# Performance work log

Measured on AMD Instinct MI355X. Metric: run time of the kernel, lower is better.

The kernel has to match this reference:

```python
import jax, jax.numpy as jnp
import numpy as np
import math

B, T, D, N = 4, 2048, 1024, 16
HD = D // N
SCALE = math.sqrt(D)  # source scales by sqrt(d_key) = sqrt(full model dim)
BIG = 1e9

def setup_inputs() -> dict:
    key = jax.random.key(0)
    ks = jax.random.split(key, 11)
    s = 1.0 / math.sqrt(D)
    return {
        "query": jax.random.normal(ks[0], (B, T, D), jnp.float32),
        "key": jax.random.normal(ks[1], (B, T, D), jnp.float32),
        "value": jax.random.normal(ks[2], (B, T, D), jnp.float32),
        "wq_w": jax.random.normal(ks[3], (D, D), jnp.float32) * s,
        "wq_b": jnp.zeros((D,), jnp.float32),
        "wk_w": jax.random.normal(ks[4], (D, D), jnp.float32) * s,
        "wk_b": jnp.zeros((D,), jnp.float32),
        "wv_w": jax.random.normal(ks[5], (D, D), jnp.float32) * s,
        "wv_b": jnp.zeros((D,), jnp.float32),
        "wo_w": jax.random.normal(ks[6], (D, D), jnp.float32) * s,
        "wo_b": jnp.zeros((D,), jnp.float32),
    }

def reference(query, key, value, wq_w, wq_b, wk_w, wk_b, wv_w, wv_b, wo_w, wo_b):
    # projections (torch Linear equiv; weights stored as (in,out))
    q = query @ wq_w + wq_b
    k = key @ wk_w + wk_b
    v = value @ wv_w + wv_b
    # split heads: (B,T,D) -> (B,N,T,HD)
    def split(x):
        return x.reshape(B, T, N, HD).transpose(0, 2, 1, 3)
    q, k, v = split(q), split(k), split(v)
    # dot products (source does elementwise mul+sum == einsum)
    scores = jnp.einsum('bnqd,bnkd->bnqk', q, k)
    # only_attend_front: subtract 1e9 on strict upper triangle
    tri = jnp.triu(jnp.ones((T, T), scores.dtype), 1) * BIG
    scores = scores - tri
    logits = scores / SCALE
    probs = jax.nn.softmax(logits, axis=-1)
    # zero rows where every position is masked (source trick)
    alive = ((scores <= -BIG / 2).sum(-1, keepdims=True) < T).astype(probs.dtype)
    probs = probs * alive
    out = jnp.einsum('bnqk,bnkd->bnqd', probs, v)  # (B,N,T,HD)
    out = out.transpose(0, 2, 1, 3).reshape(B, T, D)
    return out @ wo_w + wo_b
```

## Files before the change

### kernel.cpp

```cpp
#include <hip/hip_runtime.h>
#include <hip/hip_bf16.h>

#define BB 4
#define TT 2048
#define DD 1024
#define NHEAD 16
#define HDIM 64

typedef __bf16 v8bf __attribute__((ext_vector_type(8)));
typedef __bf16 v4bf __attribute__((ext_vector_type(4)));
typedef float  v4f  __attribute__((ext_vector_type(4)));

#define C2SCALE 0.04508422376f

__device__ __forceinline__ void gl2lds16(const void* g, void* l) {
  __builtin_amdgcn_global_load_lds(
      (__attribute__((address_space(1))) const void*)g,
      (__attribute__((address_space(3))) void*)l, 16, 0, 0);
}

__global__ __launch_bounds__(256) void prep(
    const float* __restrict__ qsrc, const float* __restrict__ ksrc,
    const float* __restrict__ vsrc,
    const float* __restrict__ w0, const float* __restrict__ w1,
    const float* __restrict__ w2, const float* __restrict__ w3,
    __bf16* __restrict__ qdst, __bf16* __restrict__ kdst,
    __bf16* __restrict__ vdst,
    __bf16* __restrict__ t0, __bf16* __restrict__ t1,
    __bf16* __restrict__ t2, __bf16* __restrict__ t3) {
  constexpr int STR = 72;
  __shared__ __bf16 sh[64 * STR];
  int bx = blockIdx.x, tid = threadIdx.x;
  if (bx < 12288) {
    const float* src = bx < 4096 ? qsrc : bx < 8192 ? ksrc : vsrc;
    __bf16* dst = bx < 4096 ? qdst : bx < 8192 ? kdst : vdst;
    int i = (bx & 4095) * 256 + tid;
    const float4* s = (const float4*)src + (size_t)i * 2;
    float4 f0 = s[0], f1 = s[1];
    v8bf v;
    v[0] = (__bf16)f0.x; v[1] = (__bf16)f0.y; v[2] = (__bf16)f0.z; v[3] = (__bf16)f0.w;
    v[4] = (__bf16)f1.x; v[5] = (__bf16)f1.y; v[6] = (__bf16)f1.z; v[7] = (__bf16)f1.w;
    *(v8bf*)(dst + (size_t)i * 8) = v;
  } else {
    int idx = bx - 12288;
    int z = idx >> 8;
    const float* W = z == 0 ? w0 : z == 1 ? w1 : z == 2 ? w2 : w3;
    __bf16* Wt = z == 0 ? t0 : z == 1 ? t1 : z == 2 ? t2 : t3;
    int n0 = (idx & 15) * 64, k0 = ((idx >> 4) & 15) * 64;
#pragma unroll
    for (int p = 0; p < 4; ++p) {
      int c = tid + p * 256;
      int r = c >> 4, off = (c & 15) * 4;
      float4 f = *(const float4*)(W + (size_t)(k0 + r) * DD + n0 + off);
      __bf16* d = &sh[r * STR + off];
      d[0] = (__bf16)f.x; d[1] = (__bf16)f.y; d[2] = (__bf16)f.z; d[3] = (__bf16)f.w;
    }
    __syncthreads();
#pragma unroll
    for (int p = 0; p < 2; ++p) {
      int c = tid + p * 256;
      int nr = c >> 3, koff = (c & 7) * 8;
      v8bf v;
#pragma unroll
      for (int j = 0; j < 8; ++j) v[j] = sh[(koff + j) * STR + nr];
      *(v8bf*)(Wt + (size_t)(n0 + nr) * DD + k0 + koff) = v;
    }
  }
}

__device__ __forceinline__ void gemm_core(const __bf16* __restrict__ A,
                                          const __bf16* __restrict__ Wt,
                                          int m0, int n0,
                                          __bf16* ash, __bf16* bsh,
                                          int wave, int lane, int quad, int l15,
                                          v4f acc[4][4]) {
  int wm = (wave & 1) * 64, wn = (wave >> 1) * 64;
  for (int k0 = 0; k0 < DD; k0 += 64) {
    __syncthreads();
#pragma unroll
    for (int i = 0; i < 4; ++i) {
      int c = wave * 256 + i * 64 + lane;
      int row = c >> 3, g = (c & 7) ^ (row & 7);
      gl2lds16(A + (size_t)(m0 + row) * DD + k0 + g * 8, ash + wave * 2048 + i * 512);
      gl2lds16(Wt + (size_t)(n0 + row) * DD + k0 + g * 8, bsh + wave * 2048 + i * 512);
    }
    __syncthreads();
#pragma unroll
    for (int ks = 0; ks < 2; ++ks) {
      int sw = (((ks * 4 + quad) ^ (l15 & 7))) * 8;
      v8bf a[4], b[4];
#pragma unroll
      for (int jm = 0; jm < 4; ++jm) a[jm] = *(v8bf*)&ash[(wm + jm * 16 + l15) * 64 + sw];
#pragma unroll
      for (int jn = 0; jn < 4; ++jn) b[jn] = *(v8bf*)&bsh[(wn + jn * 16 + l15) * 64 + sw];
#pragma unroll
      for (int jm = 0; jm < 4; ++jm)
#pragma unroll
        for (int jn = 0; jn < 4; ++jn)
          acc[jm][jn] = __builtin_amdgcn_mfma_f32_16x16x32_bf16(a[jm], b[jn], acc[jm][jn], 0, 0, 0);
    }
  }
}

__device__ __forceinline__ void swz_tiles(int& m0, int& n0) {
  int lin = blockIdx.x + 8 * blockIdx.y;
  int c = lin & 7, t = lin >> 3;
  n0 = (t & 7) * 128;
  m0 = (c + ((t >> 3) << 3)) * 128;
}

__global__ __launch_bounds__(256) void gemm_qkv(
    const __bf16* __restrict__ Qc, const __bf16* __restrict__ Kc,
    const __bf16* __restrict__ Vc,
    const __bf16* __restrict__ wqT, const __bf16* __restrict__ wkT,
    const __bf16* __restrict__ wvT,
    const float* __restrict__ qb, const float* __restrict__ kb,
    const float* __restrict__ vb,
    __bf16* __restrict__ Qp, __bf16* __restrict__ Kp, __bf16* __restrict__ VTb) {
  __shared__ __bf16 ash[128 * 64];
  __shared__ __bf16 bsh[128 * 64];
  int z = blockIdx.z;
  const __bf16* A  = z == 0 ? Qc : z == 1 ? Kc : Vc;
  const __bf16* Wt = z == 0 ? wqT : z == 1 ? wkT : wvT;
  const float* bias = z == 0 ? qb : z == 1 ? kb : vb;
  int tid = threadIdx.x, wave = tid >> 6, lane = tid & 63;
  int quad = lane >> 4, l15 = lane & 15;
  int m0, n0;
  swz_tiles(m0, n0);
  int wm = (wave & 1) * 64, wn = (wave >> 1) * 64;
  v4f acc[4][4];
#pragma unroll
  for (int jm = 0; jm < 4; ++jm)
#pragma unroll
    for (int jn = 0; jn < 4; ++jn) acc[jm][jn] = (v4f){0.f, 0.f, 0.f, 0.f};

  gemm_core(A, Wt, m0, n0, ash, bsh, wave, lane, quad, l15, acc);

  if (z == 2) {
    int b = m0 >> 11;
    int tbase = (m0 & 2047) + wm;
#pragma unroll
    for (int jn = 0; jn < 4; ++jn) {
      int col = n0 + wn + jn * 16 + l15;
      float bv = bias[col];
      __bf16* rowp = VTb + ((size_t)(b * 16 + (col >> 6)) * 64 + (col & 63)) * TT;
#pragma unroll
      for (int jm = 0; jm < 4; ++jm) {
        v4bf o;
#pragma unroll
        for (int r = 0; r < 4; ++r) o[r] = (__bf16)(acc[jm][jn][r] + bv);
        *(v4bf*)(rowp + tbase + jm * 16 + quad * 4) = o;
      }
    }
  } else {
    __bf16* C = z == 0 ? Qp : Kp;
    float scale = z == 0 ? C2SCALE : 1.0f;
#pragma unroll
    for (int jn = 0; jn < 4; ++jn) {
      int col = n0 + wn + jn * 16 + l15;
      float bv = bias[col];
#pragma unroll
      for (int jm = 0; jm < 4; ++jm) {
#pragma unroll
        for (int r = 0; r < 4; ++r) {
          int row = m0 + wm + jm * 16 + quad * 4 + r;
          C[(size_t)row * DD + col] = (__bf16)((acc[jm][jn][r] + bv) * scale);
        }
      }
    }
  }
}

__global__ __launch_bounds__(256) void gemm_out(const __bf16* __restrict__ A,
                                                const __bf16* __restrict__ Wt,
                                                const float* __restrict__ bias,
                                                float* __restrict__ C) {
  __shared__ __bf16 ash[128 * 64];
  __shared__ __bf16 bsh[128 * 64];
  int tid = threadIdx.x, wave = tid >> 6, lane = tid & 63;
  int quad = lane >> 4, l15 = lane & 15;
  int m0, n0;
  swz_tiles(m0, n0);
  int wm = (wave & 1) * 64, wn = (wave >> 1) * 64;
  v4f acc[4][4];
#pragma unroll
  for (int jm = 0; jm < 4; ++jm)
#pragma unroll
    for (int jn = 0; jn < 4; ++jn) acc[jm][jn] = (v4f){0.f, 0.f, 0.f, 0.f};

  gemm_core(A, Wt, m0, n0, ash, bsh, wave, lane, quad, l15, acc);

#pragma unroll
  for (int jn = 0; jn < 4; ++jn) {
    int col = n0 + wn + jn * 16 + l15;
    float bv = bias[col];
#pragma unroll
    for (int jm = 0; jm < 4; ++jm) {
#pragma unroll
      for (int r = 0; r < 4; ++r) {
        int row = m0 + wm + jm * 16 + quad * 4 + r;
        C[(size_t)row * DD + col] = acc[jm][jn][r] + bv;
      }
    }
  }
}

__global__ __launch_bounds__(256) void attn_bal(const __bf16* __restrict__ Q,
                                                const __bf16* __restrict__ K,
                                                const __bf16* __restrict__ VT,
                                                __bf16* __restrict__ O) {
  __shared__ __bf16 ksh[2][64 * 64];
  __shared__ __bf16 vsh[2][64 * 64];
  __shared__ __bf16 psh[128 * 64];
  int tid = threadIdx.x, wave = tid >> 6, lane = tid & 63;
  int quad = lane >> 4, l15 = lane & 15;
  int swz = l15 & 7;
  int lin = blockIdx.x + 8 * blockIdx.y;
  int c = lin & 7, t = lin >> 3;
  int xq = t & 7;
  int bh = c + ((t >> 3) << 3);
  int b = bh >> 4, h = bh & 15;
  const __bf16* Qb = Q + (size_t)(b * TT) * DD + h * HDIM;
  const __bf16* Kb = K + (size_t)(b * TT) * DD + h * HDIM;
  const __bf16* Vb = VT + (size_t)bh * HDIM * TT;
  __bf16* Ob = O + (size_t)(b * TT) * DD + h * HDIM;

  v8bf ones;
#pragma unroll
  for (int j = 0; j < 8; ++j) ones[j] = (__bf16)1.0f;

  for (int phase = 0; phase < 2; ++phase) {
    int qi = phase ? 15 - xq : xq;
    int q0 = qi * 128;
    int ktiles = 2 * qi + 2;

#pragma unroll
    for (int i = 0; i < 4; ++i) {
      int cc = wave * 256 + i * 64 + lane;
      int row = cc >> 3, g = (cc & 7) ^ (row & 7);
      gl2lds16(Qb + (size_t)(q0 + row) * DD + g * 8, psh + wave * 2048 + i * 512);
    }
#pragma unroll
    for (int i = 0; i < 2; ++i) {
      int cc = wave * 128 + i * 64 + lane;
      int row = cc >> 3, g = (cc & 7) ^ (row & 7);
      gl2lds16(Kb + (size_t)row * DD + g * 8, &ksh[0][wave * 1024 + i * 512]);
      gl2lds16(Vb + (size_t)row * TT + g * 8, &vsh[0][wave * 1024 + i * 512]);
    }
    __builtin_amdgcn_s_waitcnt(0);
    __syncthreads();

    v8bf qf[2][2];
#pragma unroll
    for (int set = 0; set < 2; ++set)
#pragma unroll
      for (int ks = 0; ks < 2; ++ks)
        qf[set][ks] = *(v8bf*)&psh[(wave * 32 + set * 16 + l15) * 64 + ((ks * 4 + quad) ^ swz) * 8];

    int qg[2] = {q0 + wave * 32 + l15, q0 + wave * 32 + 16 + l15};
    v4f oacc[2][4], lracc[2];
#pragma unroll
    for (int set = 0; set < 2; ++set) {
      lracc[set] = (v4f){0.f, 0.f, 0.f, 0.f};
#pragma unroll
      for (int jm = 0; jm < 4; ++jm) oacc[set][jm] = (v4f){0.f, 0.f, 0.f, 0.f};
    }

    int pbuf = 0;
    for (int kt = 0; kt < ktiles; ++kt) {
      if (kt + 1 < ktiles) {
        int k0n = (kt + 1) * 64;
#pragma unroll
        for (int i = 0; i < 2; ++i) {
          int cc = wave * 128 + i * 64 + lane;
          int row = cc >> 3, g = (cc & 7) ^ (row & 7);
          gl2lds16(Kb + (size_t)(k0n + row) * DD + g * 8, &ksh[pbuf ^ 1][wave * 1024 + i * 512]);
          gl2lds16(Vb + (size_t)row * TT + k0n + g * 8, &vsh[pbuf ^ 1][wave * 1024 + i * 512]);
        }
      }
      int k0 = kt * 64;
      const __bf16* kshp = &ksh[pbuf][0];
      const __bf16* vshp = &vsh[pbuf][0];

      v4f s[2][4];
#pragma unroll
      for (int set = 0; set < 2; ++set)
#pragma unroll
        for (int jf = 0; jf < 4; ++jf) s[set][jf] = (v4f){0.f, 0.f, 0.f, 0.f};
#pragma unroll
      for (int ks = 0; ks < 2; ++ks) {
        int sw = ((ks * 4 + quad) ^ swz) * 8;
#pragma unroll
        for (int jf = 0; jf < 4; ++jf) {
          v8bf kf = *(v8bf*)&kshp[(jf * 16 + l15) * 64 + sw];
          s[0][jf] = __builtin_amdgcn_mfma_f32_16x16x32_bf16(kf, qf[0][ks], s[0][jf], 0, 0, 0);
          s[1][jf] = __builtin_amdgcn_mfma_f32_16x16x32_bf16(kf, qf[1][ks], s[1][jf], 0, 0, 0);
        }
      }

      bool diag = (kt >= 2 * qi);
#pragma unroll
      for (int set = 0; set < 2; ++set) {
        int qrow = wave * 32 + set * 16 + l15;
        __bf16* prow = &psh[qrow * 64];
#pragma unroll
        for (int jf = 0; jf < 4; ++jf) {
          v4bf pk;
#pragma unroll
          for (int r = 0; r < 4; ++r) {
            float p = __builtin_amdgcn_exp2f(s[set][jf][r]);
            if (diag) {
              int kg = k0 + jf * 16 + quad * 4 + r;
              if (kg > qg[set]) p = 0.f;
            }
            pk[r] = (__bf16)p;
          }
          int chunk = jf * 2 + (quad >> 1);
          *(v4bf*)&prow[(chunk ^ swz) * 8 + (quad & 1) * 4] = pk;
        }
      }

#pragma unroll
      for (int ks = 0; ks < 2; ++ks) {
        int sw = ((ks * 4 + quad) ^ swz) * 8;
        v8bf pb0 = *(v8bf*)&psh[(wave * 32 + l15) * 64 + sw];
        v8bf pb1 = *(v8bf*)&psh[(wave * 32 + 16 + l15) * 64 + sw];
        lracc[0] = __builtin_amdgcn_mfma_f32_16x16x32_bf16(ones, pb0, lracc[0], 0, 0, 0);
        lracc[1] = __builtin_amdgcn_mfma_f32_16x16x32_bf16(ones, pb1, lracc[1], 0, 0, 0);
#pragma unroll
        for (int jm = 0; jm < 4; ++jm) {
          v8bf vf = *(v8bf*)&vshp[(jm * 16 + l15) * 64 + sw];
          oacc[0][jm] = __builtin_amdgcn_mfma_f32_16x16x32_bf16(vf, pb0, oacc[0][jm], 0, 0, 0);
          oacc[1][jm] = __builtin_amdgcn_mfma_f32_16x16x32_bf16(vf, pb1, oacc[1][jm], 0, 0, 0);
        }
      }

      __builtin_amdgcn_s_waitcnt(0);
      __syncthreads();
      pbuf ^= 1;
    }

#pragma unroll
    for (int set = 0; set < 2; ++set) {
      float inv = 1.0f / lracc[set][0];
      int q = q0 + wave * 32 + set * 16 + l15;
#pragma unroll
      for (int jm = 0; jm < 4; ++jm) {
        v4bf o;
#pragma unroll
        for (int r = 0; r < 4; ++r) o[r] = (__bf16)(oacc[set][jm][r] * inv);
        *(v4bf*)(Ob + (size_t)q * DD + jm * 16 + quad * 4) = o;
      }
    }
  }
}

extern "C" void kernel_launch(void* const* d_in, const int* in_sizes, int n_in,
                              void* d_out, int out_size, void* d_ws, size_t ws_size,
                              hipStream_t stream) {
  const float* query = (const float*)d_in[0];
  const float* key_  = (const float*)d_in[1];
  const float* value = (const float*)d_in[2];
  const float* wq_w = (const float*)d_in[3];
  const float* wq_b = (const float*)d_in[4];
  const float* wk_w = (const float*)d_in[5];
  const float* wk_b = (const float*)d_in[6];
  const float* wv_w = (const float*)d_in[7];
  const float* wv_b = (const float*)d_in[8];
  const float* wo_w = (const float*)d_in[9];
  const float* wo_b = (const float*)d_in[10];

  char* ws = (char*)d_ws;
  const size_t MB = (size_t)1 << 20;
  __bf16* wqT = (__bf16*)(ws + 0 * MB);
  __bf16* wkT = (__bf16*)(ws + 2 * MB);
  __bf16* wvT = (__bf16*)(ws + 4 * MB);
  __bf16* woT = (__bf16*)(ws + 6 * MB);
  __bf16* Qc  = (__bf16*)(ws + 8 * MB);
  __bf16* Kc  = (__bf16*)(ws + 24 * MB);
  __bf16* Vc  = (__bf16*)(ws + 40 * MB);
  __bf16* Qp  = (__bf16*)(ws + 56 * MB);
  __bf16* Kp  = (__bf16*)(ws + 72 * MB);
  __bf16* VTb = (__bf16*)(ws + 88 * MB);
  __bf16* Ab  = (__bf16*)(ws + 8 * MB);
  float* out = (float*)d_out;

  dim3 tb(256);
  prep<<<dim3(13312), tb, 0, stream>>>(query, key_, value, wq_w, wk_w, wv_w, wo_w,
                                       Qc, Kc, Vc, wqT, wkT, wvT, woT);
  gemm_qkv<<<dim3(8, 64, 3), tb, 0, stream>>>(Qc, Kc, Vc, wqT, wkT, wvT,
                                              wq_b, wk_b, wv_b, Qp, Kp, VTb);
  attn_bal<<<dim3(8, 64), tb, 0, stream>>>(Qp, Kp, VTb, Ab);
  gemm_out<<<dim3(8, 64), tb, 0, stream>>>(Ab, woT, wo_b, out);
}
```

Measured before the change: 315.7 us.

## Replace projection GEMMs with 256x256-tile 8-wave pipelined GEMM kernel

Both the QKV and output projection GEMMs now use one new kernel with 256x256 output tiles, 512 threads and double-buffered 128KB dynamic LDS. Global-to-LDS loads for the next k-tiles are split into quarters and interleaved with MFMA phases, using explicit vmcnt waits, barriers and setprio. The aim is to raise arithmetic intensity and overlap memory with compute compared with the old single-buffered 128x128 kernel. In exchange the output GEMM launches only 128 workgroups, which may underfill the GPU, and the larger tiles use much more LDS, which limits occupancy.

```diff
diff --git a/kernel.cpp b/kernel.cpp
--- a/kernel.cpp
+++ b/kernel.cpp
@@ -6,6 +6,7 @@
 #define DD 1024
 #define NHEAD 16
 #define HDIM 64
+#define NKT 16
 
 typedef __bf16 v8bf __attribute__((ext_vector_type(8)));
 typedef __bf16 v4bf __attribute__((ext_vector_type(4)));
@@ -68,141 +69,167 @@
   }
 }
 
-__device__ __forceinline__ void gemm_core(const __bf16* __restrict__ A,
-                                          const __bf16* __restrict__ Wt,
-                                          int m0, int n0,
-                                          __bf16* ash, __bf16* bsh,
-                                          int wave, int lane, int quad, int l15,
-                                          v4f acc[4][4]) {
-  int wm = (wave & 1) * 64, wn = (wave >> 1) * 64;
-  for (int k0 = 0; k0 < DD; k0 += 64) {
-    __syncthreads();
-#pragma unroll
-    for (int i = 0; i < 4; ++i) {
-      int c = wave * 256 + i * 64 + lane;
-      int row = c >> 3, g = (c & 7) ^ (row & 7);
-      gl2lds16(A + (size_t)(m0 + row) * DD + k0 + g * 8, ash + wave * 2048 + i * 512);
-      gl2lds16(Wt + (size_t)(n0 + row) * DD + k0 + g * 8, bsh + wave * 2048 + i * 512);
-    }
-    __syncthreads();
-#pragma unroll
-    for (int ks = 0; ks < 2; ++ks) {
-      int sw = (((ks * 4 + quad) ^ (l15 & 7))) * 8;
-      v8bf a[4], b[4];
-#pragma unroll
-      for (int jm = 0; jm < 4; ++jm) a[jm] = *(v8bf*)&ash[(wm + jm * 16 + l15) * 64 + sw];
-#pragma unroll
-      for (int jn = 0; jn < 4; ++jn) b[jn] = *(v8bf*)&bsh[(wn + jn * 16 + l15) * 64 + sw];
-#pragma unroll
-      for (int jm = 0; jm < 4; ++jm)
-#pragma unroll
-        for (int jn = 0; jn < 4; ++jn)
-          acc[jm][jn] = __builtin_amdgcn_mfma_f32_16x16x32_bf16(a[jm], b[jn], acc[jm][jn], 0, 0, 0);
-    }
+__global__ __launch_bounds__(512, 2) void gemm8p(
+    const __bf16* __restrict__ A0p, const __bf16* __restrict__ A1p,
+    const __bf16* __restrict__ A2p,
+    const __bf16* __restrict__ W0p, const __bf16* __restrict__ W1p,
+    const __bf16* __restrict__ W2p,
+    const float* __restrict__ b0p, const float* __restrict__ b1p,
+    const float* __restrict__ b2p,
+    __bf16* __restrict__ Qp, __bf16* __restrict__ Kp,
+    __bf16* __restrict__ VTb, float* __restrict__ Cf, int mode) {
+  extern __shared__ __bf16 lds[];
+  int tid = threadIdx.x, wave = tid >> 6, lane = tid & 63;
+  int quad = lane >> 4, l15 = lane & 15, swz = l15 & 7;
+  int wm2 = wave >> 2, wn4 = wave & 3;
+  int lin = blockIdx.x;
+  int qx = gridDim.x >> 3;
+  int wg = (lin >> 3) + (lin & 7) * qx;
+  int z = wg >> 7, t = wg & 127;
+  int m0 = (t >> 2) * 256, n0 = (t & 3) * 256;
+  const __bf16* __restrict__ A  = z == 0 ? A0p : z == 1 ? A1p : A2p;
+  const __bf16* __restrict__ Wt = z == 0 ? W0p : z == 1 ? W1p : W2p;
+  const float* __restrict__ bias = z == 0 ? b0p : z == 1 ? b1p : b2p;
+
+  v4f acc[8][4];
+#pragma unroll
+  for (int mi = 0; mi < 8; ++mi)
+#pragma unroll
+    for (int ni = 0; ni < 4; ++ni) acc[mi][ni] = (v4f){0.f, 0.f, 0.f, 0.f};
+
+#define STAGE(XP, x0, base, h, kt) do {                                     \
+  int k0s = (kt) * 64;                                                      \
+_Pragma("unroll")                                                           \
+  for (int w = 0; w < 2; ++w) {                                             \
+    int idx = w * 512 + tid;                                                \
+    int srow = (h) * 128 + (idx >> 3);                                      \
+    int g = (idx & 7) ^ (srow & 7);                                         \
+    gl2lds16((XP) + (size_t)((x0) + srow) * DD + k0s + g * 8,               \
+             lds + (base) + (h) * 8192 + idx * 8);                          \
+  }                                                                         \
+} while (0)
+
+#define LD_A(d, mh) do {                                                    \
+_Pragma("unroll")                                                           \
+  for (int ks = 0; ks < 2; ++ks)                                            \
+_Pragma("unroll")                                                           \
+    for (int jm = 0; jm < 4; ++jm)                                          \
+      afr[ks][jm] = *(const v8bf*)&lds[(d) * 32768 +                        \
+          (wm2 * 64 + (mh) * 128 + jm * 16 + l15) * 64 +                    \
+          ((ks * 4 + quad) ^ swz) * 8];                                     \
+} while (0)
+
+#define LD_B(d, nh) do {                                                    \
+_Pragma("unroll")                                                           \
+  for (int ks = 0; ks < 2; ++ks)                                            \
+_Pragma("unroll")                                                           \
+    for (int jn = 0; jn < 2; ++jn)                                          \
+      bfr[nh][ks][jn] = *(const v8bf*)&lds[(d) * 32768 + 16384 +            \
+          (wn4 * 32 + (nh) * 128 + jn * 16 + l15) * 64 +                    \
+          ((ks * 4 + quad) ^ swz) * 8];                                     \
+} while (0)
+
+#define SYNC_MID(VM) do {                                                   \
+  asm volatile("s_waitcnt vmcnt(" #VM ")" ::: "memory");                    \
+  __builtin_amdgcn_s_barrier();                                             \
+  asm volatile("s_waitcnt lgkmcnt(0)" ::: "memory");                        \
+} while (0)
+
+#define MFMA16(mh, nh) do {                                                 \
+  __builtin_amdgcn_s_setprio(1);                                            \
+_Pragma("unroll")                                                           \
+  for (int ks = 0; ks < 2; ++ks)                                            \
+_Pragma("unroll")                                                           \
+    for (int jm = 0; jm < 4; ++jm)                                          \
+_Pragma("unroll")                                                           \
+      for (int jn = 0; jn < 2; ++jn)                                        \
+        acc[(mh) * 4 + jm][(nh) * 2 + jn] =                                 \
+            __builtin_amdgcn_mfma_f32_16x16x32_bf16(                        \
+                afr[ks][jm], bfr[nh][ks][jn],                               \
+                acc[(mh) * 4 + jm][(nh) * 2 + jn], 0, 0, 0);                \
+  __builtin_amdgcn_s_setprio(0);                                            \
+  __builtin_amdgcn_s_barrier();                                             \
+} while (0)
+
+#define TILE(d, jt) do {                                                    \
+  v8bf afr[2][4]; v8bf bfr[2][2][2];                                        \
+                                                  \
+  LD_A(d, 0); LD_B(d, 0);                                                   \
+  if ((jt) + 1 < NKT) STAGE(A, m0, ((d) ^ 1) * 32768, 1, (jt) + 1);         \
+  SYNC_MID(6); MFMA16(0, 0);                                                \
+                                                        \
+  LD_B(d, 1);                                                               \
+  if ((jt) + 1 < NKT) STAGE(Wt, n0, ((d) ^ 1) * 32768 + 16384, 1, (jt) + 1);\
+  SYNC_MID(6); MFMA16(0, 1);                                                \
+                                                        \
+  LD_A(d, 1);                                                               \
+  if ((jt) + 2 < NKT) STAGE(A, m0, (d) * 32768, 0, (jt) + 2);               \
+  SYNC_MID(6); MFMA16(1, 0);                                                \
+                                                        \
+  if ((jt) + 2 < NKT) STAGE(Wt, n0, (d) * 32768 + 16384, 0, (jt) + 2);      \
+  SYNC_MID(6); MFMA16(1, 1);                                                \
+} while (0)
+
+  STAGE(A, m0, 0, 0, 0);
+  STAGE(Wt, n0, 16384, 0, 0);
+  STAGE(A, m0, 0, 1, 0);
+  STAGE(Wt, n0, 16384, 1, 0);
+  STAGE(A, m0, 32768, 0, 1);
+  STAGE(Wt, n0, 32768 + 16384, 0, 1);
+  asm volatile("s_waitcnt vmcnt(8)" ::: "memory");
+  __builtin_amdgcn_s_barrier();
+
+  for (int j2 = 0; j2 < 7; ++j2) {
+    TILE(0, j2 * 2);
+    TILE(1, j2 * 2 + 1);
   }
-}
-
-__device__ __forceinline__ void swz_tiles(int& m0, int& n0) {
-  int lin = blockIdx.x + 8 * blockIdx.y;
-  int c = lin & 7, t = lin >> 3;
-  n0 = (t & 7) * 128;
-  m0 = (c + ((t >> 3) << 3)) * 128;
-}
-
-__global__ __launch_bounds__(256) void gemm_qkv(
-    const __bf16* __restrict__ Qc, const __bf16* __restrict__ Kc,
-    const __bf16* __restrict__ Vc,
-    const __bf16* __restrict__ wqT, const __bf16* __restrict__ wkT,
-    const __bf16* __restrict__ wvT,
-    const float* __restrict__ qb, const float* __restrict__ kb,
-    const float* __restrict__ vb,
-    __bf16* __restrict__ Qp, __bf16* __restrict__ Kp, __bf16* __restrict__ VTb) {
-  __shared__ __bf16 ash[128 * 64];
-  __shared__ __bf16 bsh[128 * 64];
-  int z = blockIdx.z;
-  const __bf16* A  = z == 0 ? Qc : z == 1 ? Kc : Vc;
-  const __bf16* Wt = z == 0 ? wqT : z == 1 ? wkT : wvT;
-  const float* bias = z == 0 ? qb : z == 1 ? kb : vb;
-  int tid = threadIdx.x, wave = tid >> 6, lane = tid & 63;
-  int quad = lane >> 4, l15 = lane & 15;
-  int m0, n0;
-  swz_tiles(m0, n0);
-  int wm = (wave & 1) * 64, wn = (wave >> 1) * 64;
-  v4f acc[4][4];
-#pragma unroll
-  for (int jm = 0; jm < 4; ++jm)
-#pragma unroll
-    for (int jn = 0; jn < 4; ++jn) acc[jm][jn] = (v4f){0.f, 0.f, 0.f, 0.f};
-
-  gemm_core(A, Wt, m0, n0, ash, bsh, wave, lane, quad, l15, acc);
-
-  if (z == 2) {
-    int b = m0 >> 11;
-    int tbase = (m0 & 2047) + wm;
-#pragma unroll
-    for (int jn = 0; jn < 4; ++jn) {
-      int col = n0 + wn + jn * 16 + l15;
-      float bv = bias[col];
+  TILE(0, 14);
+  asm volatile("s_waitcnt vmcnt(0)" ::: "memory");
+  __builtin_amdgcn_s_barrier();
+  TILE(1, 15);
+
+#pragma unroll
+  for (int ni = 0; ni < 4; ++ni) {
+    int col = n0 + wn4 * 32 + (ni >> 1) * 128 + (ni & 1) * 16 + l15;
+    float bv = bias[col];
+    if (mode) {
+#pragma unroll
+      for (int mi = 0; mi < 8; ++mi) {
+        int row = m0 + wm2 * 64 + (mi >> 2) * 128 + (mi & 3) * 16 + quad * 4;
+#pragma unroll
+        for (int r = 0; r < 4; ++r)
+          Cf[(size_t)(row + r) * DD + col] = acc[mi][ni][r] + bv;
+      }
+    } else if (z == 2) {
+      int b = m0 >> 11;
       __bf16* rowp = VTb + ((size_t)(b * 16 + (col >> 6)) * 64 + (col & 63)) * TT;
-#pragma unroll
-      for (int jm = 0; jm < 4; ++jm) {
+      int tb0 = (m0 & 2047) + wm2 * 64;
+#pragma unroll
+      for (int mi = 0; mi < 8; ++mi) {
+        int tb = tb0 + (mi >> 2) * 128 + (mi & 3) * 16 + quad * 4;
         v4bf o;
 #pragma unroll
-        for (int r = 0; r < 4; ++r) o[r] = (__bf16)(acc[jm][jn][r] + bv);
-        *(v4bf*)(rowp + tbase + jm * 16 + quad * 4) = o;
-      }
-    }
-  } else {
-    __bf16* C = z == 0 ? Qp : Kp;
-    float scale = z == 0 ? C2SCALE : 1.0f;
-#pragma unroll
-    for (int jn = 0; jn < 4; ++jn) {
-      int col = n0 + wn + jn * 16 + l15;
-      float bv = bias[col];
-#pragma unroll
-      for (int jm = 0; jm < 4; ++jm) {
-#pragma unroll
-        for (int r = 0; r < 4; ++r) {
-          int row = m0 + wm + jm * 16 + quad * 4 + r;
-          C[(size_t)row * DD + col] = (__bf16)((acc[jm][jn][r] + bv) * scale);
-        }
+        for (int r = 0; r < 4; ++r) o[r] = (__bf16)(acc[mi][ni][r] + bv);
+        *(v4bf*)(rowp + tb) = o;
+      }
+    } else {
+      __bf16* C = z == 0 ? Qp : Kp;
+      float scale = z == 0 ? C2SCALE : 1.0f;
+#pragma unroll
+      for (int mi = 0; mi < 8; ++mi) {
+        int row = m0 + wm2 * 64 + (mi >> 2) * 128 + (mi & 3) * 16 + quad * 4;
+#pragma unroll
+        for (int r = 0; r < 4; ++r)
+          C[(size_t)(row + r) * DD + col] = (__bf16)((acc[mi][ni][r] + bv) * scale);
       }
     }
   }
-}
-
-__global__ __launch_bounds__(256) void gemm_out(const __bf16* __restrict__ A,
-                                                const __bf16* __restrict__ Wt,
-                                                const float* __restrict__ bias,
-                                                float* __restrict__ C) {
-  __shared__ __bf16 ash[128 * 64];
-  __shared__ __bf16 bsh[128 * 64];
-  int tid = threadIdx.x, wave = tid >> 6, lane = tid & 63;
-  int quad = lane >> 4, l15 = lane & 15;
-  int m0, n0;
-  swz_tiles(m0, n0);
-  int wm = (wave & 1) * 64, wn = (wave >> 1) * 64;
-  v4f acc[4][4];
-#pragma unroll
-  for (int jm = 0; jm < 4; ++jm)
-#pragma unroll
-    for (int jn = 0; jn < 4; ++jn) acc[jm][jn] = (v4f){0.f, 0.f, 0.f, 0.f};
-
-  gemm_core(A, Wt, m0, n0, ash, bsh, wave, lane, quad, l15, acc);
-
-#pragma unroll
-  for (int jn = 0; jn < 4; ++jn) {
-    int col = n0 + wn + jn * 16 + l15;
-    float bv = bias[col];
-#pragma unroll
-    for (int jm = 0; jm < 4; ++jm) {
-#pragma unroll
-      for (int r = 0; r < 4; ++r) {
-        int row = m0 + wm + jm * 16 + quad * 4 + r;
-        C[(size_t)row * DD + col] = acc[jm][jn][r] + bv;
-      }
-    }
-  }
+#undef TILE
+#undef MFMA16
+#undef SYNC_MID
+#undef LD_B
+#undef LD_A
+#undef STAGE
 }
 
 __global__ __launch_bounds__(256) void attn_bal(const __bf16* __restrict__ Q,
@@ -385,11 +412,20 @@
   __bf16* Ab  = (__bf16*)(ws + 8 * MB);
   float* out = (float*)d_out;
 
+  static int attr_done = 0;
+  if (!attr_done) {
+    hipFuncSetAttribute((const void*)gemm8p,
+                        hipFuncAttributeMaxDynamicSharedMemorySize, 131072);
+    attr_done = 1;
+  }
+
   dim3 tb(256);
   prep<<<dim3(13312), tb, 0, stream>>>(query, key_, value, wq_w, wk_w, wv_w, wo_w,
                                        Qc, Kc, Vc, wqT, wkT, wvT, woT);
-  gemm_qkv<<<dim3(8, 64, 3), tb, 0, stream>>>(Qc, Kc, Vc, wqT, wkT, wvT,
-                                              wq_b, wk_b, wv_b, Qp, Kp, VTb);
+  gemm8p<<<dim3(384), dim3(512), 131072, stream>>>(
+      Qc, Kc, Vc, wqT, wkT, wvT, wq_b, wk_b, wv_b, Qp, Kp, VTb, nullptr, 0);
   attn_bal<<<dim3(8, 64), tb, 0, stream>>>(Qp, Kp, VTb, Ab);
-  gemm_out<<<dim3(8, 64), tb, 0, stream>>>(Ab, woT, wo_b, out);
+  gemm8p<<<dim3(128), dim3(512), 131072, stream>>>(
+      Ab, Ab, Ab, woT, woT, woT, wo_b, wo_b, wo_b, nullptr, nullptr, nullptr,
+      out, 1);
 }
```

Result: slower. 349.8 us (+10.8%).
